# Performance work log

Hardware: AMD Instinct MI355X
Metric: run time of the kernel (lower is better)

Reference implementation:

```python
import jax, jax.numpy as jnp
import numpy as np

N = 20000      # nodes
E = 640000     # edges
F_IN = 256     # num_features
HID = 256      # hidden_dim
EMB = 256      # embedding_dim
OUT = 1        # output_dim


def setup_inputs() -> dict:
    key = jax.random.key(0)
    ks = jax.random.split(key, 8)
    g = lambda k, shp: jax.random.normal(k, shp, dtype=jnp.float32) / np.sqrt(shp[0]).astype(np.float32)
    return {
        "x": jax.random.normal(ks[0], (N, F_IN), dtype=jnp.float32),
        "edge_index": jax.random.randint(ks[1], (2, E), 0, N, dtype=jnp.int64),
        "W1": g(ks[2], (F_IN, HID)),
        "b1": jnp.zeros((HID,), jnp.float32),
        "Wh": g(ks[3], (HID, HID)),
        "bh": jnp.zeros((HID,), jnp.float32),
        "W2": g(ks[4], (HID, EMB)),
        "b2": jnp.zeros((EMB,), jnp.float32),
        "Wout": g(ks[5], (EMB, OUT)),
        "bout": jnp.zeros((OUT,), jnp.float32),
    }


def reference(x, edge_index, W1, b1, Wh, bh, W2, b2, Wout, bout):
    n = x.shape[0]
    # PyG GCNConv: add self-loops, symmetric normalization D^-1/2 (A+I) D^-1/2
    loop = jnp.arange(n, dtype=edge_index.dtype)
    row = jnp.concatenate([edge_index[0], loop])  # source j
    col = jnp.concatenate([edge_index[1], loop])  # target i
    deg = jax.ops.segment_sum(jnp.ones(row.shape[0], x.dtype), col, num_segments=n)
    dinv = jnp.where(deg > 0, jax.lax.rsqrt(deg), 0.0)
    norm = dinv[row] * dinv[col]  # [E+N]

    def conv(h, W, b):
        hw = h @ W                                   # dense GEMM [n, d_out]
        msg = hw[row] * norm[:, None]                # gather + scale
        return jax.ops.segment_sum(msg, col, num_segments=n) + b  # scatter-add

    h = jax.nn.relu(conv(x, W1, b1))   # gcn1 (dropout_rate=0 -> identity)
    h = jax.nn.relu(conv(h, Wh, bh))   # hidden GCNConv
    h = conv(h, W2, b2)                # gcn2 -> embedding
    out = h @ Wout + bout              # Decoder_linear
    return (out, h)
```

## Files before the change

### kernel.cpp

```cpp
#include <hip/hip_runtime.h>
#include <hip/hip_bf16.h>

#define NN 20000
#define EE 640000

typedef __attribute__((ext_vector_type(8))) short bf16x8;
typedef __attribute__((ext_vector_type(4))) float f32x4;

__device__ __forceinline__ ushort f2b(float f) {
    __hip_bfloat16 h = __float2bfloat16(f);
    return *(ushort*)&h;
}
__device__ __forceinline__ float b2f(ushort u) {
    __hip_bfloat16 h = *(__hip_bfloat16*)&u;
    return __bfloat162float(h);
}

__device__ __forceinline__ void acc8(float m, bf16x8 v, float* acc) {
    union { bf16x8 v; unsigned u[4]; } t;
    t.v = v;
    #pragma unroll
    for (int k = 0; k < 4; ++k) {
        acc[2 * k]     = fmaf(m, __uint_as_float(t.u[k] << 16), acc[2 * k]);
        acc[2 * k + 1] = fmaf(m, __uint_as_float(t.u[k] & 0xffff0000u), acc[2 * k + 1]);
    }
}

__device__ __forceinline__ void gload16(const ushort* g, ushort* l) {
    __builtin_amdgcn_global_load_lds(
        (const __attribute__((address_space(1))) void*)g,
        (__attribute__((address_space(3))) void*)l, 16, 0, 0);
}


__global__ void init_cnt_kernel(int* __restrict__ cnt, int n) {
    int i = blockIdx.x * 256 + threadIdx.x;
    if (i < n) cnt[i] = 0;
}

__global__ void hist_kernel(const int* __restrict__ col, int* __restrict__ cnt, int e) {
    int i = blockIdx.x * 256 + threadIdx.x;
    if (i < e) atomicAdd(&cnt[col[i]], 1);
}

__device__ __forceinline__ int block_exscan(int v) {
    __shared__ int wsum[4];
    int tid = threadIdx.x, lane = tid & 63, w = tid >> 6;
    int x = v;
    #pragma unroll
    for (int d = 1; d < 64; d <<= 1) {
        int y = __shfl_up(x, d, 64);
        if (lane >= d) x += y;
    }
    if (lane == 63) wsum[w] = x;
    __syncthreads();
    if (tid == 0) {
        int s = 0;
        #pragma unroll
        for (int k = 0; k < 4; ++k) { int t = wsum[k]; wsum[k] = s; s += t; }
    }
    __syncthreads();
    return wsum[w] + x - v;
}

__global__ __launch_bounds__(256) void scan_p1_kernel(const int* __restrict__ cnt,
                                                      int* __restrict__ offs,
                                                      int* __restrict__ bsum,
                                                      float* __restrict__ dinv, int n) {
    int i = blockIdx.x * 256 + threadIdx.x;
    int v = (i < n) ? cnt[i] : 0;
    int e = block_exscan(v);
    if (i < n) {
        offs[i] = e;
        dinv[i] = rsqrtf((float)(v + 1));
    }
    if (threadIdx.x == 255) bsum[blockIdx.x] = e + v;
}

__global__ __launch_bounds__(256) void scan_p2_kernel(int* __restrict__ bsum, int nblk) {
    int t = threadIdx.x;
    int v = (t < nblk) ? bsum[t] : 0;
    int e = block_exscan(v);
    if (t < nblk) bsum[t] = e;
}

__global__ __launch_bounds__(256) void scan_p3_kernel(int* __restrict__ offs,
                                                      const int* __restrict__ bsum,
                                                      int* __restrict__ cursor, int n) {
    int i = blockIdx.x * 256 + threadIdx.x;
    if (i < n) {
        int o = offs[i] + bsum[blockIdx.x];
        offs[i] = o;
        cursor[i] = o;
    }
}

__global__ void scatter_kernel(const int* __restrict__ row, const int* __restrict__ col,
                               const float* __restrict__ dinv, int* __restrict__ cursor,
                               unsigned* __restrict__ pq, int e) {
    int i = blockIdx.x * 256 + threadIdx.x;
    if (i >= e) return;
    int s = row[i], d = col[i];
    int pos = atomicAdd(&cursor[d], 1);
    unsigned nb = f2b(dinv[s] * dinv[d]);
    pq[pos] = (nb << 16) | (unsigned)s;
}

__global__ __launch_bounds__(256) void prep_kernel(
    const float* __restrict__ W1, const float* __restrict__ Wh,
    const float* __restrict__ W2, ushort* __restrict__ Wt,
    const float* __restrict__ x, ushort* __restrict__ xb,
    const float* __restrict__ bout, float* __restrict__ outv, int n) {
    int bid = blockIdx.x;
    if (bid < 768) {
        const float* W = (bid < 256) ? W1 : ((bid < 512) ? Wh : W2);
        ushort* dst = Wt + (size_t)(bid >> 8) * 256 * 512;
        int col = bid & 255;
        #pragma unroll
        for (int kv = threadIdx.x; kv < 512; kv += 256) {
            int k = kv & 255;
            float w = W[(size_t)k * 256 + col];
            ushort hi = f2b(w);
            dst[(size_t)col * 512 + kv] = (kv < 256) ? hi : f2b(w - b2f(hi));
        }
    } else if (bid < 768 + 2500) {
        int i = (bid - 768) * 256 + threadIdx.x;
        if (i < n * 32) {
            float4 a = ((const float4*)x)[2 * i];
            float4 b = ((const float4*)x)[2 * i + 1];
            union { bf16x8 v; ushort s[8]; } o;
            o.s[0] = f2b(a.x); o.s[1] = f2b(a.y); o.s[2] = f2b(a.z); o.s[3] = f2b(a.w);
            o.s[4] = f2b(b.x); o.s[5] = f2b(b.y); o.s[6] = f2b(b.z); o.s[7] = f2b(b.w);
            ((bf16x8*)xb)[i] = o.v;
        }
    } else {
        int i = (bid - 3268) * 256 + threadIdx.x;
        if (i < n) outv[i] = bout[0];
    }
}

__global__ __launch_bounds__(256) void gemm_mfma_kernel(
    const ushort* __restrict__ A, const ushort* __restrict__ Wt,
    ushort* __restrict__ G, int n) {
    __shared__ ushort Ast[2][128][64];
    __shared__ ushort Bst[2][128][64];
    int tid = threadIdx.x;
    int lane = tid & 63, wid = tid >> 6;
    int rowbase = blockIdx.x * 128;
    int colbase = blockIdx.y * 64;

    f32x4 zero = {0.f, 0.f, 0.f, 0.f};
    f32x4 acc[2][4];
    #pragma unroll
    for (int m = 0; m < 2; ++m)
        #pragma unroll
        for (int nn = 0; nn < 4; ++nn) acc[m][nn] = zero;

    int rsub = lane >> 3, sl = lane & 7;
    const ushort* asrc[4];
    const ushort* bsrc[4];
    #pragma unroll
    for (int q = 0; q < 4; ++q) {
        int rin = wid * 32 + q * 8 + rsub;
        int c = sl ^ (rin & 7);
        int gr = min(rowbase + rin, n - 1);
        asrc[q] = A + (size_t)gr * 256 + c * 8;
        int col_r = rin & 63;
        int part = rin >> 6;
        bsrc[q] = Wt + (size_t)(colbase + col_r) * 512 + part * 256 + c * 8;
    }

    auto stage = [&](int kt, int buf) {
        int kv0 = kt * 64;
        #pragma unroll
        for (int q = 0; q < 4; ++q)
            gload16(asrc[q] + kv0, &Ast[buf][wid * 32 + q * 8][0]);
        #pragma unroll
        for (int q = 0; q < 4; ++q)
            gload16(bsrc[q] + kv0, &Bst[buf][wid * 32 + q * 8][0]);
    };

    stage(0, 0);
    for (int kt = 0; kt < 4; ++kt) {
        int cur = kt & 1;
        if (kt < 3) {
            stage(kt + 1, cur ^ 1);
            asm volatile("s_waitcnt vmcnt(8)" ::: "memory");
        } else {
            asm volatile("s_waitcnt vmcnt(0)" ::: "memory");
        }
        __builtin_amdgcn_s_barrier();
        #pragma unroll
        for (int kk = 0; kk < 2; ++kk) {
            int clog = kk * 4 + (lane >> 4);
            bf16x8 af[2], bfh[4], bfl[4];
            #pragma unroll
            for (int m = 0; m < 2; ++m) {
                int row = wid * 32 + m * 16 + (lane & 15);
                af[m] = *(const bf16x8*)&Ast[cur][row][(clog ^ (row & 7)) * 8];
            }
            #pragma unroll
            for (int nn = 0; nn < 4; ++nn) {
                int rowh = nn * 16 + (lane & 15);
                int rowl = rowh + 64;
                bfh[nn] = *(const bf16x8*)&Bst[cur][rowh][(clog ^ (rowh & 7)) * 8];
                bfl[nn] = *(const bf16x8*)&Bst[cur][rowl][(clog ^ (rowl & 7)) * 8];
            }
            #pragma unroll
            for (int m = 0; m < 2; ++m)
                #pragma unroll
                for (int nn = 0; nn < 4; ++nn) {
                    acc[m][nn] = __builtin_amdgcn_mfma_f32_16x16x32_bf16(
                        af[m], bfh[nn], acc[m][nn], 0, 0, 0);
                    acc[m][nn] = __builtin_amdgcn_mfma_f32_16x16x32_bf16(
                        af[m], bfl[nn], acc[m][nn], 0, 0, 0);
                }
        }
        __builtin_amdgcn_s_barrier();
    }

    #pragma unroll
    for (int nn = 0; nn < 4; ++nn) {
        int col = colbase + nn * 16 + (lane & 15);
        #pragma unroll
        for (int m = 0; m < 2; ++m) {
            int grow0 = rowbase + wid * 32 + m * 16 + ((lane >> 4) << 2);
            f32x4 v = acc[m][nn];
            #pragma unroll
            for (int rr = 0; rr < 4; ++rr) {
                int row = grow0 + rr;
                if (row < n)
                    G[(size_t)row * 256 + col] = f2b(v[rr]);
            }
        }
    }
}

template<bool FINAL>
__global__ __launch_bounds__(256) void agg_kernel(
    const ushort* __restrict__ g,
    const int* __restrict__ offs, const int* __restrict__ cnt,
    const unsigned* __restrict__ pq,
    const float* __restrict__ dinv,
    const float* __restrict__ bias,
    ushort* __restrict__ hb,
    float* __restrict__ h3,
    const float* __restrict__ Wout, float* __restrict__ outv,
    int n) {
    int chunk = blockIdx.x & 3;
    int lane = threadIdx.x & 63;
    int half = lane >> 5;
    int esub = (lane >> 3) & 3;
    int fsub = lane & 7;
    int node = (blockIdx.x >> 2) * 8 + (threadIdx.x >> 6) * 2 + half;
    const ushort* base = g + chunk * 64 + fsub * 8;

    int beg = offs[node], num = cnt[node];
    float acc[8] = {};

    unsigned q[8];
    #pragma unroll
    for (int u = 0; u < 8; ++u) {
        int i = u * 4 + esub;
        q[u] = pq[i < num ? beg + i : 0];
    }

    for (int j = 0; j < num; j += 32) {
        bf16x8 v[8];
        #pragma unroll
        for (int u = 0; u < 8; ++u)
            v[u] = *(const bf16x8*)(base + (size_t)(q[u] & 0xffffu) * 256);
        unsigned p[8];
        #pragma unroll
        for (int u = 0; u < 8; ++u) {
            int i = j + 32 + u * 4 + esub;
            p[u] = pq[i < num ? beg + i : 0];
        }
        #pragma unroll
        for (int u = 0; u < 8; ++u) {
            float m = (j + u * 4 + esub) < num ? __uint_as_float(q[u] & 0xffff0000u) : 0.f;
            acc8(m, v[u], acc);
        }
        #pragma unroll
        for (int u = 0; u < 8; ++u) q[u] = p[u];
    }

    #pragma unroll
    for (int d = 8; d < 32; d <<= 1)
        #pragma unroll
        for (int k = 0; k < 8; ++k)
            acc[k] += __shfl_xor(acc[k], d, 64);

    if (esub == 0) {
        float di = dinv[node];
        bf16x8 sv = *(const bf16x8*)(base + (size_t)node * 256);
        acc8(di * di, sv, acc);
        int feat = chunk * 64 + fsub * 8;
        float4 b0 = *(const float4*)(bias + feat);
        float4 b1 = *(const float4*)(bias + feat + 4);
        acc[0] += b0.x; acc[1] += b0.y; acc[2] += b0.z; acc[3] += b0.w;
        acc[4] += b1.x; acc[5] += b1.y; acc[6] += b1.z; acc[7] += b1.w;
        if (!FINAL) {
            union { bf16x8 v; ushort s[8]; } o;
            #pragma unroll
            for (int k = 0; k < 8; ++k)
                o.s[k] = f2b(fmaxf(acc[k], 0.f));
            *(bf16x8*)(hb + (size_t)node * 256 + feat) = o.v;
        } else {
            float4 o0 = {acc[0], acc[1], acc[2], acc[3]};
            float4 o1 = {acc[4], acc[5], acc[6], acc[7]};
            *(float4*)(h3 + (size_t)node * 256 + feat)     = o0;
            *(float4*)(h3 + (size_t)node * 256 + feat + 4) = o1;
            float4 w0 = *(const float4*)(Wout + feat);
            float4 w1 = *(const float4*)(Wout + feat + 4);
            float dot = acc[0] * w0.x + acc[1] * w0.y + acc[2] * w0.z + acc[3] * w0.w
                      + acc[4] * w1.x + acc[5] * w1.y + acc[6] * w1.z + acc[7] * w1.w;
            #pragma unroll
            for (int d = 1; d < 8; d <<= 1)
                dot += __shfl_xor(dot, d, 64);
            if (fsub == 0) atomicAdd(&outv[node], dot);
        }
    }
}

extern "C" void kernel_launch(void* const* d_in, const int* in_sizes, int n_in,
                              void* d_out, int out_size, void* d_ws, size_t ws_size,
                              hipStream_t stream) {
    const int n = NN, e = EE;
    const float* x    = (const float*)d_in[0];
    const int*   eidx = (const int*)d_in[1];
    const float* W1   = (const float*)d_in[2];
    const float* b1   = (const float*)d_in[3];
    const float* Wh   = (const float*)d_in[4];
    const float* bh   = (const float*)d_in[5];
    const float* W2   = (const float*)d_in[6];
    const float* b2   = (const float*)d_in[7];
    const float* Wout = (const float*)d_in[8];
    const float* bout = (const float*)d_in[9];
    const int* row = eidx;
    const int* col = eidx + e;

    char* ws = (char*)d_ws;
    int*      cnt     = (int*)ws;      ws += (size_t)n * 4;
    int*      offs    = (int*)ws;      ws += (size_t)n * 4;
    int*      cursor  = (int*)ws;      ws += (size_t)n * 4;
    float*    dinv    = (float*)ws;    ws += (size_t)n * 4;
    int*      bsum    = (int*)ws;      ws += (size_t)256 * 4;
    unsigned* pq      = (unsigned*)ws; ws += (size_t)e * 4;
    ushort*   xb      = (ushort*)ws;   ws += (size_t)n * 256 * 2;
    ushort*   hb      = (ushort*)ws;   ws += (size_t)n * 256 * 2;
    ushort*   g2      = (ushort*)ws;   ws += (size_t)n * 256 * 2;
    ushort*   wt      = (ushort*)ws;   ws += (size_t)3 * 256 * 512 * 2;
    ushort* wt1 = wt;
    ushort* wt2 = wt + (size_t)256 * 512;
    ushort* wt3 = wt + (size_t)2 * 256 * 512;

    float* outv = (float*)d_out;
    float* h3   = (float*)d_out + n;

    int nb_n = (n + 255) / 256;
    int nb_e = (e + 255) / 256;

    init_cnt_kernel<<<nb_n, 256, 0, stream>>>(cnt, n);
    hist_kernel<<<nb_e, 256, 0, stream>>>(col, cnt, e);
    scan_p1_kernel<<<nb_n, 256, 0, stream>>>(cnt, offs, bsum, dinv, n);
    scan_p2_kernel<<<1, 256, 0, stream>>>(bsum, nb_n);
    scan_p3_kernel<<<nb_n, 256, 0, stream>>>(offs, bsum, cursor, n);
    scatter_kernel<<<nb_e, 256, 0, stream>>>(row, col, dinv, cursor, pq, e);

    prep_kernel<<<768 + 2500 + 79, 256, 0, stream>>>(W1, Wh, W2, wt, x, xb, bout, outv, n);

    int agrid = (n / 8) * 4;
    dim3 ggrid((n + 127) / 128, 4);

    gemm_mfma_kernel<<<ggrid, 256, 0, stream>>>(xb, wt1, g2, n);
    agg_kernel<false><<<agrid, 256, 0, stream>>>(
        g2, offs, cnt, pq, dinv, b1, hb, nullptr, nullptr, nullptr, n);
    gemm_mfma_kernel<<<ggrid, 256, 0, stream>>>(hb, wt2, g2, n);
    agg_kernel<false><<<agrid, 256, 0, stream>>>(
        g2, offs, cnt, pq, dinv, bh, hb, nullptr, nullptr, nullptr, n);
    gemm_mfma_kernel<<<ggrid, 256, 0, stream>>>(hb, wt3, g2, n);
    agg_kernel<true><<<agrid, 256, 0, stream>>>(
        g2, offs, cnt, pq, dinv, b2, nullptr, h3, Wout, outv, n);
}
```

Measured before the change: 236.4 us.

## Fuse setup kernels and shrink aggregation unroll with packed FMA

Zeroing of the count array moves into the prep kernel, and the two scan passes merge into one kernel where each block redoes the small block-sum scan. Together these cut two launches. The aggregation loop drops from 8 to 4 edges per lane per iteration and uses two-wide float vector FMAs, which should lower register pressure and allow packed FMA instructions. The cost is less memory-level parallelism per thread in the gather, and every block now repeats the tiny scan of block sums.

After: 211.1 us. 1.12x faster.

```diff
diff --git a/kernel.cpp b/kernel.cpp
--- a/kernel.cpp
+++ b/kernel.cpp
@@ -6,6 +6,7 @@
 
 typedef __attribute__((ext_vector_type(8))) short bf16x8;
 typedef __attribute__((ext_vector_type(4))) float f32x4;
+typedef __attribute__((ext_vector_type(2))) float f32x2;
 
 __device__ __forceinline__ ushort f2b(float f) {
     __hip_bfloat16 h = __float2bfloat16(f);
@@ -16,13 +17,15 @@
     return __bfloat162float(h);
 }
 
-__device__ __forceinline__ void acc8(float m, bf16x8 v, float* acc) {
+__device__ __forceinline__ void acc8p(float m, bf16x8 v, f32x2* acc) {
     union { bf16x8 v; unsigned u[4]; } t;
     t.v = v;
+    f32x2 mm = {m, m};
     #pragma unroll
     for (int k = 0; k < 4; ++k) {
-        acc[2 * k]     = fmaf(m, __uint_as_float(t.u[k] << 16), acc[2 * k]);
-        acc[2 * k + 1] = fmaf(m, __uint_as_float(t.u[k] & 0xffff0000u), acc[2 * k + 1]);
+        f32x2 f = { __uint_as_float(t.u[k] << 16),
+                    __uint_as_float(t.u[k] & 0xffff0000u) };
+        acc[k] = __builtin_elementwise_fma(mm, f, acc[k]);
     }
 }
 
@@ -32,11 +35,6 @@
         (__attribute__((address_space(3))) void*)l, 16, 0, 0);
 }
 
-
-__global__ void init_cnt_kernel(int* __restrict__ cnt, int n) {
-    int i = blockIdx.x * 256 + threadIdx.x;
-    if (i < n) cnt[i] = 0;
-}
 
 __global__ void hist_kernel(const int* __restrict__ col, int* __restrict__ cnt, int e) {
     int i = blockIdx.x * 256 + threadIdx.x;
@@ -77,19 +75,19 @@
     if (threadIdx.x == 255) bsum[blockIdx.x] = e + v;
 }
 
-__global__ __launch_bounds__(256) void scan_p2_kernel(int* __restrict__ bsum, int nblk) {
+__global__ __launch_bounds__(256) void scan_p23_kernel(int* __restrict__ offs,
+                                                       const int* __restrict__ bsum,
+                                                       int* __restrict__ cursor,
+                                                       int n, int nblk) {
+    __shared__ int base_s;
     int t = threadIdx.x;
     int v = (t < nblk) ? bsum[t] : 0;
     int e = block_exscan(v);
-    if (t < nblk) bsum[t] = e;
-}
-
-__global__ __launch_bounds__(256) void scan_p3_kernel(int* __restrict__ offs,
-                                                      const int* __restrict__ bsum,
-                                                      int* __restrict__ cursor, int n) {
-    int i = blockIdx.x * 256 + threadIdx.x;
+    if (t == blockIdx.x) base_s = e;
+    __syncthreads();
+    int i = blockIdx.x * 256 + t;
     if (i < n) {
-        int o = offs[i] + bsum[blockIdx.x];
+        int o = offs[i] + base_s;
         offs[i] = o;
         cursor[i] = o;
     }
@@ -110,7 +108,8 @@
     const float* __restrict__ W1, const float* __restrict__ Wh,
     const float* __restrict__ W2, ushort* __restrict__ Wt,
     const float* __restrict__ x, ushort* __restrict__ xb,
-    const float* __restrict__ bout, float* __restrict__ outv, int n) {
+    const float* __restrict__ bout, float* __restrict__ outv,
+    int* __restrict__ cnt, int n) {
     int bid = blockIdx.x;
     if (bid < 768) {
         const float* W = (bid < 256) ? W1 : ((bid < 512) ? Wh : W2);
@@ -133,9 +132,12 @@
             o.s[4] = f2b(b.x); o.s[5] = f2b(b.y); o.s[6] = f2b(b.z); o.s[7] = f2b(b.w);
             ((bf16x8*)xb)[i] = o.v;
         }
-    } else {
+    } else if (bid < 768 + 2500 + 79) {
         int i = (bid - 3268) * 256 + threadIdx.x;
         if (i < n) outv[i] = bout[0];
+    } else {
+        int i = (bid - 3347) * 256 + threadIdx.x;
+        if (i < n) cnt[i] = 0;
     }
 }
 
@@ -256,65 +258,67 @@
     const ushort* base = g + chunk * 64 + fsub * 8;
 
     int beg = offs[node], num = cnt[node];
-    float acc[8] = {};
-
-    unsigned q[8];
-    #pragma unroll
-    for (int u = 0; u < 8; ++u) {
-        int i = u * 4 + esub;
-        q[u] = pq[i < num ? beg + i : 0];
-    }
-
-    for (int j = 0; j < num; j += 32) {
-        bf16x8 v[8];
-        #pragma unroll
-        for (int u = 0; u < 8; ++u)
-            v[u] = *(const bf16x8*)(base + (size_t)(q[u] & 0xffffu) * 256);
-        unsigned p[8];
-        #pragma unroll
-        for (int u = 0; u < 8; ++u) {
-            int i = j + 32 + u * 4 + esub;
-            p[u] = pq[i < num ? beg + i : 0];
-        }
-        #pragma unroll
-        for (int u = 0; u < 8; ++u) {
-            float m = (j + u * 4 + esub) < num ? __uint_as_float(q[u] & 0xffff0000u) : 0.f;
-            acc8(m, v[u], acc);
-        }
-        #pragma unroll
-        for (int u = 0; u < 8; ++u) q[u] = p[u];
+    f32x2 acc[4] = {};
+
+    unsigned q0 = pq[(esub)      < num ? beg + esub      : 0];
+    unsigned q1 = pq[(4 + esub)  < num ? beg + 4 + esub  : 0];
+    unsigned q2 = pq[(8 + esub)  < num ? beg + 8 + esub  : 0];
+    unsigned q3 = pq[(12 + esub) < num ? beg + 12 + esub : 0];
+
+    for (int j = 0; j < num; j += 16) {
+        int jn = j + 16;
+        unsigned p0 = pq[(jn + esub)      < num ? beg + jn + esub      : 0];
+        unsigned p1 = pq[(jn + 4 + esub)  < num ? beg + jn + 4 + esub  : 0];
+        unsigned p2 = pq[(jn + 8 + esub)  < num ? beg + jn + 8 + esub  : 0];
+        unsigned p3 = pq[(jn + 12 + esub) < num ? beg + jn + 12 + esub : 0];
+
+        float m0 = (j +      esub) < num ? __uint_as_float(q0 & 0xffff0000u) : 0.f;
+        float m1 = (j + 4  + esub) < num ? __uint_as_float(q1 & 0xffff0000u) : 0.f;
+        float m2 = (j + 8  + esub) < num ? __uint_as_float(q2 & 0xffff0000u) : 0.f;
+        float m3 = (j + 12 + esub) < num ? __uint_as_float(q3 & 0xffff0000u) : 0.f;
+        bf16x8 v0 = *(const bf16x8*)(base + (size_t)(q0 & 0xffffu) * 256);
+        bf16x8 v1 = *(const bf16x8*)(base + (size_t)(q1 & 0xffffu) * 256);
+        bf16x8 v2 = *(const bf16x8*)(base + (size_t)(q2 & 0xffffu) * 256);
+        bf16x8 v3 = *(const bf16x8*)(base + (size_t)(q3 & 0xffffu) * 256);
+        acc8p(m0, v0, acc);
+        acc8p(m1, v1, acc);
+        acc8p(m2, v2, acc);
+        acc8p(m3, v3, acc);
+        q0 = p0; q1 = p1; q2 = p2; q3 = p3;
     }
 
     #pragma unroll
     for (int d = 8; d < 32; d <<= 1)
         #pragma unroll
-        for (int k = 0; k < 8; ++k)
-            acc[k] += __shfl_xor(acc[k], d, 64);
+        for (int k = 0; k < 4; ++k) {
+            acc[k][0] += __shfl_xor(acc[k][0], d, 64);
+            acc[k][1] += __shfl_xor(acc[k][1], d, 64);
+        }
 
     if (esub == 0) {
         float di = dinv[node];
         bf16x8 sv = *(const bf16x8*)(base + (size_t)node * 256);
-        acc8(di * di, sv, acc);
+        acc8p(di * di, sv, acc);
         int feat = chunk * 64 + fsub * 8;
         float4 b0 = *(const float4*)(bias + feat);
         float4 b1 = *(const float4*)(bias + feat + 4);
-        acc[0] += b0.x; acc[1] += b0.y; acc[2] += b0.z; acc[3] += b0.w;
-        acc[4] += b1.x; acc[5] += b1.y; acc[6] += b1.z; acc[7] += b1.w;
+        acc[0][0] += b0.x; acc[0][1] += b0.y; acc[1][0] += b0.z; acc[1][1] += b0.w;
+        acc[2][0] += b1.x; acc[2][1] += b1.y; acc[3][0] += b1.z; acc[3][1] += b1.w;
         if (!FINAL) {
             union { bf16x8 v; ushort s[8]; } o;
             #pragma unroll
             for (int k = 0; k < 8; ++k)
-                o.s[k] = f2b(fmaxf(acc[k], 0.f));
+                o.s[k] = f2b(fmaxf(acc[k >> 1][k & 1], 0.f));
             *(bf16x8*)(hb + (size_t)node * 256 + feat) = o.v;
         } else {
-            float4 o0 = {acc[0], acc[1], acc[2], acc[3]};
-            float4 o1 = {acc[4], acc[5], acc[6], acc[7]};
+            float4 o0 = {acc[0][0], acc[0][1], acc[1][0], acc[1][1]};
+            float4 o1 = {acc[2][0], acc[2][1], acc[3][0], acc[3][1]};
             *(float4*)(h3 + (size_t)node * 256 + feat)     = o0;
             *(float4*)(h3 + (size_t)node * 256 + feat + 4) = o1;
             float4 w0 = *(const float4*)(Wout + feat);
             float4 w1 = *(const float4*)(Wout + feat + 4);
-            float dot = acc[0] * w0.x + acc[1] * w0.y + acc[2] * w0.z + acc[3] * w0.w
-                      + acc[4] * w1.x + acc[5] * w1.y + acc[6] * w1.z + acc[7] * w1.w;
+            float dot = o0.x * w0.x + o0.y * w0.y + o0.z * w0.z + o0.w * w0.w
+                      + o1.x * w1.x + o1.y * w1.y + o1.z * w1.z + o1.w * w1.w;
             #pragma unroll
             for (int d = 1; d < 8; d <<= 1)
                 dot += __shfl_xor(dot, d, 64);
@@ -361,14 +365,13 @@
     int nb_n = (n + 255) / 256;
     int nb_e = (e + 255) / 256;
 
-    init_cnt_kernel<<<nb_n, 256, 0, stream>>>(cnt, n);
+    prep_kernel<<<768 + 2500 + 79 + 79, 256, 0, stream>>>(
+        W1, Wh, W2, wt, x, xb, bout, outv, cnt, n);
+
     hist_kernel<<<nb_e, 256, 0, stream>>>(col, cnt, e);
     scan_p1_kernel<<<nb_n, 256, 0, stream>>>(cnt, offs, bsum, dinv, n);
-    scan_p2_kernel<<<1, 256, 0, stream>>>(bsum, nb_n);
-    scan_p3_kernel<<<nb_n, 256, 0, stream>>>(offs, bsum, cursor, n);
+    scan_p23_kernel<<<nb_n, 256, 0, stream>>>(offs, bsum, cursor, n, nb_n);
     scatter_kernel<<<nb_e, 256, 0, stream>>>(row, col, dinv, cursor, pq, e);
-
-    prep_kernel<<<768 + 2500 + 79, 256, 0, stream>>>(W1, Wh, W2, wt, x, xb, bout, outv, n);
 
     int agrid = (n / 8) * 4;
     dim3 ggrid((n + 127) / 128, 4);
```
